# Kernel tuning notes

Hardware: AMD Instinct MI355X
Metric: run time of the kernel (lower is better)

## Reference

```python
import jax, jax.numpy as jnp
import numpy as np

NUM_PTS = 5      # num_points_per_it
MAX_IT = 25      # RANSAC iterations
TOL = 0.1        # inlier tolerance
G_PRIOR = 0.5    # bottom fraction of image assumed ground
VAX = 1          # vertical axis index


def get_AB(pts):
    """pts (..., 3) -> A (..., 3) = [non-vertical coords, 1], Bm (..., 1) = vertical coord."""
    Bm = pts[..., VAX:VAX + 1]
    cols = [pts[..., i:i + 1] for i in range(3) if i != VAX]
    A = jnp.concatenate(cols + [jnp.ones_like(Bm)], axis=-1)
    return A, Bm


def setup_inputs() -> dict:
    key = jax.random.key(0)
    k1, k2 = jax.random.split(key)
    B, H, W = 4, 384, 1280
    points = jax.random.normal(k1, (B, 3, H, W), dtype=jnp.float32)
    N = int(G_PRIOR * H) * W  # 245760 ground-candidate points per image
    T = NUM_PTS * MAX_IT      # 125 sampled indices per image
    rand_ind = jax.random.randint(k2, (B, T), 0, N, dtype=jnp.int32)
    return {"points": points, "rand_ind": rand_ind}


def reference(points, rand_ind):
    B, _, H, W = points.shape
    gH = int(G_PRIOR * H)
    N = gH * W
    # ground candidates: bottom half of image -> (B, N, 3)
    gp = points[:, :, H - gH:, :].reshape(B, 3, N).transpose(0, 2, 1)
    # gather RANSAC samples -> (B*MAX_IT, NUM_PTS, 3), b-major order (matches torch stack+reshape)
    sampled = jnp.take_along_axis(gp, rand_ind[..., None], axis=1).reshape(B * MAX_IT, NUM_PTS, 3)
    # least-squares plane fit per hypothesis: w = inv(A^T A + 1e-6) A^T b  (scalar 1e-6 added to ALL entries, faithful to torch)
    A, Bm = get_AB(sampled)
    At = jnp.swapaxes(A, 1, 2)
    ws = jnp.linalg.inv(At @ A + 1e-6) @ At @ Bm  # (B*MAX_IT, 3, 1)
    # NOTE: original code pairs ws (b-major) with points.repeat(max_it,1,1) (it-major);
    # we replicate that pairing exactly for faithfulness.
    ps = jnp.tile(gp, (MAX_IT, 1, 1))  # (MAX_IT*B, N, 3)
    Ap, Bp = get_AB(ps)
    abs_dist = jnp.abs(Ap @ ws - Bp).reshape(B, MAX_IT, N)
    # inlier voting + best hypothesis per image
    fit = (abs_dist < TOL).astype(jnp.float32).mean(axis=2)  # (B, MAX_IT)
    best = jnp.argmax(fit, axis=1)
    best_w = ws.reshape(B, MAX_IT, 3, 1)[jnp.arange(B), best]  # (B, 3, 1)
    # distance of every pixel to selected plane
    ap = points.reshape(B, 3, H * W).transpose(0, 2, 1)
    Aa, Ba = get_AB(ap)
    dist = (Aa @ best_w - Ba).transpose(0, 2, 1).reshape(B, 1, H, W)
    # forward returns detached tensors
    return jax.lax.stop_gradient(dist), jax.lax.stop_gradient(best_w)
```

## Files before the change

kernel.cpp:

```cpp
#include <hip/hip_runtime.h>


constexpr int BN      = 4;
constexpr int H       = 384;
constexpr int W       = 1280;
constexpr int HW      = H * W;
constexpr int GH      = 192;
constexpr int NPTS    = GH * W;
constexpr int MAX_IT  = 25;
constexpr int NUM_PTS = 5;
constexpr int TOTAL_P = BN * MAX_IT;

constexpr int PLANES_PB    = 25;
constexpr int CH_F4        = 512;
constexpr int CHUNKS       = (NPTS / 4) / CH_F4;
constexpr int ITERS        = CH_F4 / 256;
constexpr int PSTRIDE      = 128;
constexpr int BLOCKS_PER_B = (HW / 4) / 256;

__global__ __launch_bounds__(256) void k_count(
        const float* __restrict__ pts, const int* __restrict__ rind,
        float* __restrict__ wsf, int* __restrict__ partial) {
    __shared__ float sw[PLANES_PB][3];
    __shared__ int   spid[PLANES_PB];
    __shared__ int   sacc[PLANES_PB];
    int pb    = blockIdx.x & 3;
    int chunk = blockIdx.x >> 2;
    int tid   = threadIdx.x;
    if (tid < PLANES_PB) {
        sacc[tid] = 0;
        int s = 0, pi = 0;
        for (int b = 0; b < BN; ++b) {
            int r = ((pb - b) % BN + BN) % BN;
            for (int it = r; it < MAX_IT; it += BN) {
                if (s == tid) pi = b * MAX_IT + it;
                ++s;
            }
        }
        spid[tid] = pi;
        int fb = pi / MAX_IT, fit_it = pi % MAX_IT;
        const float* base = pts + (size_t)fb * 3 * HW + (size_t)(H - GH) * W;
        const int* ri = rind + fb * (MAX_IT * NUM_PTS) + fit_it * NUM_PTS;
        double Sxx = 0, Sxz = 0, Sx = 0, Szz = 0, Sz = 0, Sxy = 0, Szy = 0, Sy = 0;
#pragma unroll
        for (int p = 0; p < NUM_PTS; ++p) {
            int n = ri[p];
            double x = (double)base[n];
            double y = (double)base[HW + n];
            double z = (double)base[2 * HW + n];
            Sxx += x * x; Sxz += x * z; Sx += x;
            Szz += z * z; Sz += z;
            Sxy += x * y; Szy += z * y; Sy += y;
        }
        const double e = 1e-6;
        double m00 = Sxx + e, m01 = Sxz + e, m02 = Sx + e;
        double m10 = Sxz + e, m11 = Szz + e, m12 = Sz + e;
        double m20 = Sx + e,  m21 = Sz + e,  m22 = (double)NUM_PTS + e;
        double v0 = Sxy, v1 = Szy, v2 = Sy;
        double det = m00 * (m11 * m22 - m12 * m21)
                   - m01 * (m10 * m22 - m12 * m20)
                   + m02 * (m10 * m21 - m11 * m20);
        double inv = 1.0 / det;
        double d0 = v0  * (m11 * m22 - m12 * m21)
                  - m01 * (v1  * m22 - m12 * v2 )
                  + m02 * (v1  * m21 - m11 * v2 );
        double d1 = m00 * (v1  * m22 - m12 * v2 )
                  - v0  * (m10 * m22 - m12 * m20)
                  + m02 * (m10 * v2  - v1  * m20);
        double d2 = m00 * (m11 * v2  - v1  * m21)
                  - m01 * (m10 * v2  - v1  * m20)
                  + v0  * (m10 * m21 - m11 * m20);
        double w0 = d0 * inv, w1 = d1 * inv, w2 = d2 * inv;
        sw[tid][0] = (float)w0; sw[tid][1] = (float)w1; sw[tid][2] = (float)w2;
        if (chunk == 0) {
            wsf[pi * 3 + 0] = (float)w0;
            wsf[pi * 3 + 1] = (float)w1;
            wsf[pi * 3 + 2] = (float)w2;
        }
    }
    __syncthreads();
    float w0[PLANES_PB], w1[PLANES_PB], w2[PLANES_PB];
#pragma unroll
    for (int p = 0; p < PLANES_PB; ++p) {
        w0[p] = sw[p][0]; w1[p] = sw[p][1]; w2[p] = sw[p][2];
    }

    const float* base = pts + (size_t)pb * 3 * HW + (size_t)(H - GH) * W;
    const float4* px = (const float4*)base;
    const float4* py = (const float4*)(base + HW);
    const float4* pz = (const float4*)(base + 2 * HW);

    int cnt[PLANES_PB];
#pragma unroll
    for (int p = 0; p < PLANES_PB; ++p) cnt[p] = 0;

#pragma unroll
    for (int it = 0; it < ITERS; ++it) {
        int f = chunk * CH_F4 + it * 256 + tid;
        float4 x4 = px[f], y4 = py[f], z4 = pz[f];
#pragma unroll
        for (int e = 0; e < 4; ++e) {
            float x = ((const float*)&x4)[e];
            float y = ((const float*)&y4)[e];
            float z = ((const float*)&z4)[e];
#pragma unroll
            for (int p = 0; p < PLANES_PB; ++p) {
                float d = fmaf(x, w0[p], fmaf(z, w1[p], w2[p] - y));
                cnt[p] += (fabsf(d) < 0.1f) ? 1 : 0;
            }
        }
    }
#pragma unroll
    for (int p = 0; p < PLANES_PB; ++p) {
        int v = cnt[p];
        for (int off = 32; off > 0; off >>= 1) v += __shfl_down(v, off, 64);
        if ((tid & 63) == 0) atomicAdd(&sacc[p], v);
    }
    __syncthreads();
    if (tid < PLANES_PB) partial[spid[tid] * PSTRIDE + chunk] = sacc[tid];
}

__global__ __launch_bounds__(256) void k_dist(
        const float* __restrict__ pts, const float* __restrict__ wsf,
        const int* __restrict__ partial, float* __restrict__ out) {
    __shared__ int   scnt[MAX_IT];
    __shared__ float sw[3];
    int b   = blockIdx.x / BLOCKS_PER_B;
    int blk = blockIdx.x % BLOCKS_PER_B;
    int tid = threadIdx.x;
    if (tid < MAX_IT) {
        const int4* p = (const int4*)(partial + (b * MAX_IT + tid) * PSTRIDE);
        int s = 0;
#pragma unroll
        for (int c = 0; c < CHUNKS / 4; ++c) {
            int4 v = p[c];
            s += v.x + v.y + v.z + v.w;
        }
        scnt[tid] = s;
    }
    __syncthreads();
    if (tid == 0) {
        int best = 0, bc = scnt[0];
        for (int it = 1; it < MAX_IT; ++it) {
            int c = scnt[it];
            if (c > bc) { bc = c; best = it; }
        }
        int pi = b * MAX_IT + best;
        sw[0] = wsf[pi * 3 + 0];
        sw[1] = wsf[pi * 3 + 1];
        sw[2] = wsf[pi * 3 + 2];
        if (blk == 0) {
            out[(size_t)BN * HW + b * 3 + 0] = sw[0];
            out[(size_t)BN * HW + b * 3 + 1] = sw[1];
            out[(size_t)BN * HW + b * 3 + 2] = sw[2];
        }
    }
    __syncthreads();
    float w0 = sw[0], w1 = sw[1], w2 = sw[2];
    const float4* px = (const float4*)(pts + (size_t)b * 3 * HW);
    const float4* py = px + HW / 4;
    const float4* pz = py + HW / 4;
    int i = blk * 256 + tid;
    float4 x = px[i], y = py[i], z = pz[i];
    float4 r;
    r.x = w0 * x.x + w1 * z.x + w2 - y.x;
    r.y = w0 * x.y + w1 * z.y + w2 - y.y;
    r.z = w0 * x.z + w1 * z.z + w2 - y.z;
    r.w = w0 * x.w + w1 * z.w + w2 - y.w;
    ((float4*)(out + (size_t)b * HW))[i] = r;
}

extern "C" void kernel_launch(void* const* d_in, const int* in_sizes, int n_in,
                              void* d_out, int out_size, void* d_ws, size_t ws_size,
                              hipStream_t stream) {
    const float* pts  = (const float*)d_in[0];
    const int*   rind = (const int*)d_in[1];
    float* out = (float*)d_out;

    float* wsf     = (float*)d_ws;
    int*   partial = (int*)(wsf + TOTAL_P * 3 + 4);

    k_count<<<BN * CHUNKS, 256, 0, stream>>>(pts, rind, wsf, partial);
    k_dist <<<BN * BLOCKS_PER_B, 256, 0, stream>>>(pts, wsf, partial, out);
}
```

Measured before the change: 85.63 us.

## Fuse count and distance kernels via cooperative grid sync, reusing loaded points

Replaces the two-kernel sequence with a single cooperative kernel. It counts inliers, performs a grid-wide sync, then picks the best plane and writes distances. The bottom-half points stay in registers from the counting phase, and each thread preloads its top-half points before the sync, so the second pass over the point cloud in global memory is avoided. The cost is more register pressure, a grid barrier across 480 blocks that all must be co-resident, and a fallback to the old kernels if the cooperative launch fails.

```diff
diff --git a/kernel.cpp b/kernel.cpp
--- a/kernel.cpp
+++ b/kernel.cpp
@@ -1,4 +1,7 @@
 #include <hip/hip_runtime.h>
+#include <hip/hip_cooperative_groups.h>
+
+namespace cg = cooperative_groups;
 
 
 constexpr int BN      = 4;
@@ -16,7 +19,200 @@
 constexpr int CHUNKS       = (NPTS / 4) / CH_F4;
 constexpr int ITERS        = CH_F4 / 256;
 constexpr int PSTRIDE      = 128;
+constexpr int GRID         = BN * CHUNKS;
+constexpr int TOPF4_PB     = (HW / 2) / 4;
+constexpr int THREADS_TOT  = GRID * 256;
 constexpr int BLOCKS_PER_B = (HW / 4) / 256;
+
+__device__ __forceinline__ void fit_planes(
+        const float* __restrict__ pts, const int* __restrict__ rind,
+        float* __restrict__ wsf, int pb, bool publish, int tid,
+        float (*sw)[3], int* spid) {
+    int s = 0, pi = 0;
+    for (int b = 0; b < BN; ++b) {
+        int r = ((pb - b) % BN + BN) % BN;
+        for (int it = r; it < MAX_IT; it += BN) {
+            if (s == tid) pi = b * MAX_IT + it;
+            ++s;
+        }
+    }
+    spid[tid] = pi;
+    int fb = pi / MAX_IT, fit_it = pi % MAX_IT;
+    const float* base = pts + (size_t)fb * 3 * HW + (size_t)(H - GH) * W;
+    const int* ri = rind + fb * (MAX_IT * NUM_PTS) + fit_it * NUM_PTS;
+    double Sxx = 0, Sxz = 0, Sx = 0, Szz = 0, Sz = 0, Sxy = 0, Szy = 0, Sy = 0;
+#pragma unroll
+    for (int p = 0; p < NUM_PTS; ++p) {
+        int n = ri[p];
+        double x = (double)base[n];
+        double y = (double)base[HW + n];
+        double z = (double)base[2 * HW + n];
+        Sxx += x * x; Sxz += x * z; Sx += x;
+        Szz += z * z; Sz += z;
+        Sxy += x * y; Szy += z * y; Sy += y;
+    }
+    const double e = 1e-6;
+    double m00 = Sxx + e, m01 = Sxz + e, m02 = Sx + e;
+    double m10 = Sxz + e, m11 = Szz + e, m12 = Sz + e;
+    double m20 = Sx + e,  m21 = Sz + e,  m22 = (double)NUM_PTS + e;
+    double v0 = Sxy, v1 = Szy, v2 = Sy;
+    double det = m00 * (m11 * m22 - m12 * m21)
+               - m01 * (m10 * m22 - m12 * m20)
+               + m02 * (m10 * m21 - m11 * m20);
+    double inv = 1.0 / det;
+    double d0 = v0  * (m11 * m22 - m12 * m21)
+              - m01 * (v1  * m22 - m12 * v2 )
+              + m02 * (v1  * m21 - m11 * v2 );
+    double d1 = m00 * (v1  * m22 - m12 * v2 )
+              - v0  * (m10 * m22 - m12 * m20)
+              + m02 * (m10 * v2  - v1  * m20);
+    double d2 = m00 * (m11 * v2  - v1  * m21)
+              - m01 * (m10 * v2  - v1  * m20)
+              + v0  * (m10 * m21 - m11 * m20);
+    double w0 = d0 * inv, w1 = d1 * inv, w2 = d2 * inv;
+    sw[tid][0] = (float)w0; sw[tid][1] = (float)w1; sw[tid][2] = (float)w2;
+    if (publish) {
+        wsf[pi * 3 + 0] = (float)w0;
+        wsf[pi * 3 + 1] = (float)w1;
+        wsf[pi * 3 + 2] = (float)w2;
+    }
+}
+
+__global__ __launch_bounds__(256, 2) void k_fused(
+        const float* __restrict__ pts, const int* __restrict__ rind,
+        float* __restrict__ wsf, int* __restrict__ partial,
+        float* __restrict__ out) {
+    __shared__ float sw[PLANES_PB][3];
+    __shared__ int   spid[PLANES_PB];
+    __shared__ int   sacc[PLANES_PB];
+    __shared__ int   scnt[TOTAL_P];
+    __shared__ float swv[BN][3];
+
+    int pb    = blockIdx.x & 3;
+    int chunk = blockIdx.x >> 2;
+    int tid   = threadIdx.x;
+    if (tid < PLANES_PB) {
+        sacc[tid] = 0;
+        fit_planes(pts, rind, wsf, pb, chunk == 0, tid, sw, spid);
+    }
+    __syncthreads();
+    float w0[PLANES_PB], w1[PLANES_PB], w2[PLANES_PB];
+#pragma unroll
+    for (int p = 0; p < PLANES_PB; ++p) {
+        w0[p] = sw[p][0]; w1[p] = sw[p][1]; w2[p] = sw[p][2];
+    }
+
+    const float* base = pts + (size_t)pb * 3 * HW + (size_t)(H - GH) * W;
+    const float4* px = (const float4*)base;
+    const float4* py = (const float4*)(base + HW);
+    const float4* pz = (const float4*)(base + 2 * HW);
+    float4 bx[ITERS], by[ITERS], bz[ITERS];
+#pragma unroll
+    for (int it = 0; it < ITERS; ++it) {
+        int f = chunk * CH_F4 + it * 256 + tid;
+        bx[it] = px[f]; by[it] = py[f]; bz[it] = pz[f];
+    }
+    int T = blockIdx.x * 256 + tid;
+    float4 tx[2], ty[2], tz[2];
+    int tb[2], tf[2];
+#pragma unroll
+    for (int j = 0; j < 2; ++j) {
+        int idx = j * THREADS_TOT + T;
+        int bt  = idx / TOPF4_PB;
+        int ft  = idx - bt * TOPF4_PB;
+        tb[j] = bt; tf[j] = ft;
+        const float4* qx = (const float4*)(pts + (size_t)bt * 3 * HW);
+        tx[j] = qx[ft];
+        ty[j] = qx[HW / 4 + ft];
+        tz[j] = qx[2 * (HW / 4) + ft];
+    }
+
+    int cnt[PLANES_PB];
+#pragma unroll
+    for (int p = 0; p < PLANES_PB; ++p) cnt[p] = 0;
+#pragma unroll
+    for (int it = 0; it < ITERS; ++it) {
+        float4 x4 = bx[it], y4 = by[it], z4 = bz[it];
+#pragma unroll
+        for (int e = 0; e < 4; ++e) {
+            float x = ((const float*)&x4)[e];
+            float y = ((const float*)&y4)[e];
+            float z = ((const float*)&z4)[e];
+#pragma unroll
+            for (int p = 0; p < PLANES_PB; ++p) {
+                float d = fmaf(x, w0[p], fmaf(z, w1[p], w2[p] - y));
+                cnt[p] += (fabsf(d) < 0.1f) ? 1 : 0;
+            }
+        }
+    }
+#pragma unroll
+    for (int p = 0; p < PLANES_PB; ++p) {
+        int v = cnt[p];
+        for (int off = 32; off > 0; off >>= 1) v += __shfl_down(v, off, 64);
+        if ((tid & 63) == 0) atomicAdd(&sacc[p], v);
+    }
+    __syncthreads();
+    if (tid < PLANES_PB) partial[spid[tid] * PSTRIDE + chunk] = sacc[tid];
+    __threadfence();
+
+    cg::this_grid().sync();
+
+    if (tid < TOTAL_P) {
+        const int4* p = (const int4*)(partial + tid * PSTRIDE);
+        int s = 0;
+#pragma unroll
+        for (int c = 0; c < CHUNKS / 4; ++c) {
+            int4 v = p[c];
+            s += v.x + v.y + v.z + v.w;
+        }
+        scnt[tid] = s;
+    }
+    __syncthreads();
+    if (tid < BN) {
+        int b = tid;
+        int best = 0, bc = scnt[b * MAX_IT];
+        for (int it = 1; it < MAX_IT; ++it) {
+            int c = scnt[b * MAX_IT + it];
+            if (c > bc) { bc = c; best = it; }
+        }
+        int pi = b * MAX_IT + best;
+        float v0 = wsf[pi * 3 + 0], v1 = wsf[pi * 3 + 1], v2 = wsf[pi * 3 + 2];
+        swv[b][0] = v0; swv[b][1] = v1; swv[b][2] = v2;
+        if (blockIdx.x == 0) {
+            out[(size_t)BN * HW + b * 3 + 0] = v0;
+            out[(size_t)BN * HW + b * 3 + 1] = v1;
+            out[(size_t)BN * HW + b * 3 + 2] = v2;
+        }
+    }
+    __syncthreads();
+
+    {
+        float u0 = swv[pb][0], u1 = swv[pb][1], u2 = swv[pb][2];
+        float4* ob = (float4*)(out + (size_t)pb * HW + HW / 2);
+#pragma unroll
+        for (int it = 0; it < ITERS; ++it) {
+            int f = chunk * CH_F4 + it * 256 + tid;
+            float4 x4 = bx[it], y4 = by[it], z4 = bz[it];
+            float4 r;
+            r.x = fmaf(x4.x, u0, fmaf(z4.x, u1, u2 - y4.x));
+            r.y = fmaf(x4.y, u0, fmaf(z4.y, u1, u2 - y4.y));
+            r.z = fmaf(x4.z, u0, fmaf(z4.z, u1, u2 - y4.z));
+            r.w = fmaf(x4.w, u0, fmaf(z4.w, u1, u2 - y4.w));
+            ob[f] = r;
+        }
+    }
+#pragma unroll
+    for (int j = 0; j < 2; ++j) {
+        float u0 = swv[tb[j]][0], u1 = swv[tb[j]][1], u2 = swv[tb[j]][2];
+        float4 x4 = tx[j], y4 = ty[j], z4 = tz[j];
+        float4 r;
+        r.x = fmaf(x4.x, u0, fmaf(z4.x, u1, u2 - y4.x));
+        r.y = fmaf(x4.y, u0, fmaf(z4.y, u1, u2 - y4.y));
+        r.z = fmaf(x4.z, u0, fmaf(z4.z, u1, u2 - y4.z));
+        r.w = fmaf(x4.w, u0, fmaf(z4.w, u1, u2 - y4.w));
+        ((float4*)(out + (size_t)tb[j] * HW))[tf[j]] = r;
+    }
+}
 
 __global__ __launch_bounds__(256) void k_count(
         const float* __restrict__ pts, const int* __restrict__ rind,
@@ -29,54 +225,7 @@
     int tid   = threadIdx.x;
     if (tid < PLANES_PB) {
         sacc[tid] = 0;
-        int s = 0, pi = 0;
-        for (int b = 0; b < BN; ++b) {
-            int r = ((pb - b) % BN + BN) % BN;
-            for (int it = r; it < MAX_IT; it += BN) {
-                if (s == tid) pi = b * MAX_IT + it;
-                ++s;
-            }
-        }
-        spid[tid] = pi;
-        int fb = pi / MAX_IT, fit_it = pi % MAX_IT;
-        const float* base = pts + (size_t)fb * 3 * HW + (size_t)(H - GH) * W;
-        const int* ri = rind + fb * (MAX_IT * NUM_PTS) + fit_it * NUM_PTS;
-        double Sxx = 0, Sxz = 0, Sx = 0, Szz = 0, Sz = 0, Sxy = 0, Szy = 0, Sy = 0;
-#pragma unroll
-        for (int p = 0; p < NUM_PTS; ++p) {
-            int n = ri[p];
-            double x = (double)base[n];
-            double y = (double)base[HW + n];
-            double z = (double)base[2 * HW + n];
-            Sxx += x * x; Sxz += x * z; Sx += x;
-            Szz += z * z; Sz += z;
-            Sxy += x * y; Szy += z * y; Sy += y;
-        }
-        const double e = 1e-6;
-        double m00 = Sxx + e, m01 = Sxz + e, m02 = Sx + e;
-        double m10 = Sxz + e, m11 = Szz + e, m12 = Sz + e;
-        double m20 = Sx + e,  m21 = Sz + e,  m22 = (double)NUM_PTS + e;
-        double v0 = Sxy, v1 = Szy, v2 = Sy;
-        double det = m00 * (m11 * m22 - m12 * m21)
-                   - m01 * (m10 * m22 - m12 * m20)
-                   + m02 * (m10 * m21 - m11 * m20);
-        double inv = 1.0 / det;
-        double d0 = v0  * (m11 * m22 - m12 * m21)
-                  - m01 * (v1  * m22 - m12 * v2 )
-                  + m02 * (v1  * m21 - m11 * v2 );
-        double d1 = m00 * (v1  * m22 - m12 * v2 )
-                  - v0  * (m10 * m22 - m12 * m20)
-                  + m02 * (m10 * v2  - v1  * m20);
-        double d2 = m00 * (m11 * v2  - v1  * m21)
-                  - m01 * (m10 * v2  - v1  * m20)
-                  + v0  * (m10 * m21 - m11 * m20);
-        double w0 = d0 * inv, w1 = d1 * inv, w2 = d2 * inv;
-        sw[tid][0] = (float)w0; sw[tid][1] = (float)w1; sw[tid][2] = (float)w2;
-        if (chunk == 0) {
-            wsf[pi * 3 + 0] = (float)w0;
-            wsf[pi * 3 + 1] = (float)w1;
-            wsf[pi * 3 + 2] = (float)w2;
-        }
+        fit_planes(pts, rind, wsf, pb, chunk == 0, tid, sw, spid);
     }
     __syncthreads();
     float w0[PLANES_PB], w1[PLANES_PB], w2[PLANES_PB];
@@ -84,16 +233,13 @@
     for (int p = 0; p < PLANES_PB; ++p) {
         w0[p] = sw[p][0]; w1[p] = sw[p][1]; w2[p] = sw[p][2];
     }
-
     const float* base = pts + (size_t)pb * 3 * HW + (size_t)(H - GH) * W;
     const float4* px = (const float4*)base;
     const float4* py = (const float4*)(base + HW);
     const float4* pz = (const float4*)(base + 2 * HW);
-
     int cnt[PLANES_PB];
 #pragma unroll
     for (int p = 0; p < PLANES_PB; ++p) cnt[p] = 0;
-
 #pragma unroll
     for (int it = 0; it < ITERS; ++it) {
         int f = chunk * CH_F4 + it * 256 + tid;
@@ -180,6 +326,14 @@
     float* wsf     = (float*)d_ws;
     int*   partial = (int*)(wsf + TOTAL_P * 3 + 4);
 
-    k_count<<<BN * CHUNKS, 256, 0, stream>>>(pts, rind, wsf, partial);
-    k_dist <<<BN * BLOCKS_PER_B, 256, 0, stream>>>(pts, wsf, partial, out);
-}
+    void* args[5] = {(void*)&pts, (void*)&rind, (void*)&wsf, (void*)&partial,
+                     (void*)&out};
+    hipError_t err = hipLaunchCooperativeKernel((const void*)k_fused,
+                                                dim3(GRID), dim3(256),
+                                                args, 0, stream);
+    if (err != hipSuccess) {
+        (void)hipGetLastError();
+        k_count<<<GRID, 256, 0, stream>>>(pts, rind, wsf, partial);
+        k_dist <<<BN * BLOCKS_PER_B, 256, 0, stream>>>(pts, wsf, partial, out);
+    }
+}
```

After: 158.5 us. 85.1% more time.
